# Kernel tuning notes

Measured on AMD Instinct MI355X. Metric: run time of the kernel, lower is better.

Reference implementation:

```python
import jax, jax.numpy as jnp
import numpy as np

INF = 1e10
B, SQ, SK, D = 4, 2048, 2048, 1024


def setup_inputs() -> dict:
    key = jax.random.key(0)
    kq, kk, kv = jax.random.split(key, 3)
    return {
        "query": jax.random.normal(kq, (B, SQ, D), dtype=jnp.float32),
        "key": jax.random.normal(kk, (B, SK, D), dtype=jnp.float32),
        "value": jax.random.normal(kv, (B, SK, D), dtype=jnp.float32),
    }


def reference(query, key, value):
    d_key = query.shape[-1]
    scale = jnp.sqrt(jnp.asarray(d_key, dtype=query.dtype))
    # QK^T: [B, Sq, Sk]
    scores = jnp.einsum("bqd,bkd->bqk", query, key)
    # causal mask: triu(1) * INF over [Sk, Sk], take last Sq rows (matches torch)
    sk = key.shape[1]
    sq = query.shape[1]
    tri = jnp.triu(jnp.full((sk, sk), INF, dtype=scores.dtype), k=1)[-sq:]
    scores = scores - tri[None, :, :]
    # note: mask applied BEFORE scaling, as in the original
    probs = jax.nn.softmax(scores / scale, axis=-1)
    # AV: [B, Sq, D]
    return jnp.einsum("bqk,bkd->bqd", probs, value)
```

## Files before the change

kernel.cpp:

```cpp
#include <hip/hip_runtime.h>
#include <stdint.h>


#define B_SZ 4
#define SEQ 2048
#define DIM 1024
#define QBLK 32
#define KVBLK 128
#define NWAVES 8
#define PAN  ((size_t)DIM * 32)
#define KPAN ((size_t)DIM * 16)

typedef __bf16 bf16x8 __attribute__((ext_vector_type(8)));
typedef unsigned short u16x8 __attribute__((ext_vector_type(8)));
typedef unsigned short u16x4 __attribute__((ext_vector_type(4)));
typedef float f32x4 __attribute__((ext_vector_type(4)));

__device__ __forceinline__ unsigned short f2bf(float f) {
  union { float f; uint32_t u; } c; c.f = f;
  uint32_t u = c.u;
  u += 0x7FFFu + ((u >> 16) & 1u);
  return (unsigned short)(u >> 16);
}

__global__ void transpose_k_kernel(const float* __restrict__ in,
                                   unsigned short* __restrict__ out) {
  const int b   = blockIdx.z;
  const int kv0 = blockIdx.y * 16;
  const int d0  = blockIdx.x * 128;
  const int t   = threadIdx.x;
  const int kvl = t >> 4;
  const int uu  = t & 15;
  const int d   = d0 + uu * 8;
  const float* src = in + (size_t)b * SEQ * DIM + (size_t)(kv0 + kvl) * DIM + d;
  f32x4 a = *(const f32x4*)(src);
  f32x4 c = *(const f32x4*)(src + 4);
  u16x8 pk;
#pragma unroll
  for (int j = 0; j < 4; ++j) { pk[j] = f2bf(a[j]); pk[4 + j] = f2bf(c[j]); }
  *(u16x8*)(out + (size_t)b * SEQ * DIM + (size_t)blockIdx.y * KPAN
            + (size_t)(d >> 3) * 128 + kvl * 8) = pk;
}

__global__ void transpose_v_kernel(const float* __restrict__ in,
                                   unsigned short* __restrict__ out) {
  __shared__ unsigned short tile[32][33];
  const int b  = blockIdx.z;
  const int s0 = blockIdx.y * 32;
  const int d0 = blockIdx.x * 32;
  const int t  = threadIdx.x;
  const int r  = t >> 3;
  const int c4 = (t & 7) * 4;
  const size_t ibase = (size_t)b * SEQ * DIM;
  const size_t obase = (size_t)b * DIM * SEQ;

  f32x4 v = *(const f32x4*)(in + ibase + (size_t)(s0 + r) * DIM + d0 + c4);
#pragma unroll
  for (int j = 0; j < 4; ++j) tile[r][c4 + j] = f2bf(v[j]);
  __syncthreads();
  u16x4 o;
#pragma unroll
  for (int j = 0; j < 4; ++j) o[j] = tile[c4 + j][r];
  *(u16x4*)(out + obase + (size_t)(s0 >> 5) * PAN + (size_t)(d0 + r) * 32 + c4) = o;
}

__device__ __forceinline__ int imin(int a, int b) { return a < b ? a : b; }

__global__ __launch_bounds__(512, 2) void attn_part(
    const float* __restrict__ Qf, const unsigned short* __restrict__ Kp,
    const unsigned short* __restrict__ Vp, float* __restrict__ Out,
    float* __restrict__ Opart, float* __restrict__ Ml, int mode) {
  const int tid  = threadIdx.x;
  const int lane = tid & 63;
  const int wv   = tid >> 6;
  const int g    = lane >> 4;
  const int i16  = lane & 15;
  const int swz  = i16 & 7;

  const int IPX = (mode == 2) ? 80 : (mode == 1) ? 48 : 32;
  const int IPB = (mode == 2) ? 160 : (mode == 1) ? 96 : 64;
  const int item  = (blockIdx.x & 7) * IPX + (blockIdx.x >> 3);
  const int batch = item / IPB;
  const int r     = IPB - 1 - (item % IPB);

  int qt, kvlo, kvhi, slot;
  if (mode == 2) {
    if (r < 16)       { qt = r;             kvlo = 0;    kvhi = 32 * qt + 32;             slot = -1; }
    else if (r < 64)  { qt = r;             kvlo = 0;    kvhi = 512;                      slot = batch * 144 + (r - 16); }
    else if (r < 112) { qt = 16 + (r - 64); kvlo = 512;  kvhi = imin(1024, 32 * qt + 32); slot = batch * 144 + (r - 16); }
    else if (r < 144) { qt = 32 + (r - 112); kvlo = 1024; kvhi = imin(1536, 32 * qt + 32); slot = batch * 144 + (r - 16); }
    else              { qt = 48 + (r - 144); kvlo = 1536; kvhi = 32 * qt + 32;            slot = batch * 144 + (r - 16); }
  } else if (mode == 1) {
    if (r < 32)       { qt = r;             kvlo = 0;    kvhi = 32 * qt + 32;  slot = -1; }
    else if (r < 64)  { qt = 32 + (r - 32); kvlo = 0;    kvhi = 1024;          slot = batch * 64 + (r - 32); }
    else              { qt = 32 + (r - 64); kvlo = 1024; kvhi = 32 * qt + 32;  slot = batch * 64 + (r - 32); }
  } else {
    qt = r; kvlo = 0; kvhi = 32 * qt + 32; slot = -1;
  }

  const int q0 = qt * QBLK;
  const size_t boff = (size_t)batch * SEQ * DIM;

  __shared__ __align__(16) unsigned short Qs[QBLK * 1024];
  __shared__ __align__(16) unsigned short Pl[QBLK * KVBLK];
  __shared__ float pmaxT[QBLK][12];
  __shared__ float psumT[QBLK][12];

  {
    const int row = tid >> 4;
    const int s0  = tid & 15;
    const float* qrow = Qf + boff + (size_t)(q0 + row) * DIM;
#pragma unroll
    for (int k = 0; k < 8; ++k) {
      const int slot2 = s0 + 16 * k;
      f32x4 a = *(const f32x4*)(qrow + slot2 * 8);
      f32x4 b = *(const f32x4*)(qrow + slot2 * 8 + 4);
      u16x8 pk;
#pragma unroll
      for (int j = 0; j < 4; ++j) { pk[j] = f2bf(a[j]); pk[4 + j] = f2bf(b[j]); }
      *(u16x8*)(Qs + row * 1024 + (slot2 ^ (row & 7)) * 8) = pk;
    }
  }

  const f32x4 zero4 = {0.f, 0.f, 0.f, 0.f};
  f32x4 o_acc[8][2];
#pragma unroll
  for (int mt = 0; mt < 8; ++mt)
#pragma unroll
    for (int nt = 0; nt < 2; ++nt) o_acc[mt][nt] = zero4;

  float m_reg[2] = {-1e30f, -1e30f};
  float l_reg[2] = {0.f, 0.f};

  const int ntiles = (kvhi - kvlo + KVBLK - 1) >> 7;
  const unsigned short* kb = Kp + boff + (size_t)wv * KPAN + i16 * 8;
  const unsigned short* vb = Vp + boff + (size_t)(wv * 128 + i16) * 32 + g * 8;

  __syncthreads();

  for (int t = 0; t < ntiles; ++t) {
    const int kv0 = kvlo + t * KVBLK;
    const unsigned short* kt = kb + (size_t)(kv0 >> 4) * KPAN;
    const size_t vt0 = (size_t)(kv0 >> 5) * PAN;

    f32x4 sacc[2];
    sacc[0] = zero4; sacc[1] = zero4;
    bf16x8 vV0[8], vV1[8], vV2[8], vV3[8];

#pragma unroll
    for (int c = 0; c < 8; ++c) {
      if (c == 0) {
#pragma unroll
        for (int mt = 0; mt < 8; ++mt) {
          vV0[mt] = __builtin_bit_cast(bf16x8,
              *(const u16x8*)(vb + vt0 + (size_t)mt * 512));
          vV1[mt] = __builtin_bit_cast(bf16x8,
              *(const u16x8*)(vb + vt0 + PAN + (size_t)mt * 512));
        }
      }
      const unsigned short* qrb0 = Qs + (0 * 16 + i16) * 1024;
      const unsigned short* qrb1 = Qs + (1 * 16 + i16) * 1024;
      bf16x8 kf[4], qf0[4], qf1[4];
#pragma unroll
      for (int kk = 0; kk < 4; ++kk) {
        kf[kk]  = __builtin_bit_cast(bf16x8,
            *(const u16x8*)(kt + (size_t)(c * 16 + kk * 4 + g) * 128));
        qf0[kk] = __builtin_bit_cast(bf16x8, *(const u16x8*)(qrb0 + ((c * 16 + kk * 4 + g) ^ swz) * 8));
        qf1[kk] = __builtin_bit_cast(bf16x8, *(const u16x8*)(qrb1 + ((c * 16 + kk * 4 + g) ^ swz) * 8));
      }
      __builtin_amdgcn_s_setprio(1);
#pragma unroll
      for (int kk = 0; kk < 4; ++kk) {
        sacc[0] = __builtin_amdgcn_mfma_f32_16x16x32_bf16(kf[kk], qf0[kk], sacc[0], 0, 0, 0);
        sacc[1] = __builtin_amdgcn_mfma_f32_16x16x32_bf16(kf[kk], qf1[kk], sacc[1], 0, 0, 0);
      }
      __builtin_amdgcn_s_setprio(0);
    }

    float pm[2];
#pragma unroll
    for (int nt = 0; nt < 2; ++nt) {
      const int qg = q0 + nt * 16 + i16;
      const int kvbase = kv0 + wv * 16 + g * 4;
#pragma unroll
      for (int j = 0; j < 4; ++j) {
        const bool valid = (kvbase + j) <= qg;
        sacc[nt][j] = valid ? sacc[nt][j] * 0.03125f : -1e30f;
      }
      float v = fmaxf(fmaxf(sacc[nt][0], sacc[nt][1]), fmaxf(sacc[nt][2], sacc[nt][3]));
      v = fmaxf(v, __shfl_xor(v, 16));
      v = fmaxf(v, __shfl_xor(v, 32));
      pm[nt] = v;
    }
    if (lane < 32) pmaxT[(lane >> 4) * 16 + (lane & 15)][wv] = (lane < 16) ? pm[0] : pm[1];
    __syncthreads();

    float alpha[2];
#pragma unroll
    for (int nt = 0; nt < 2; ++nt) {
      const float* pr = &pmaxT[nt * 16 + i16][0];
      f32x4 a = *(const f32x4*)(pr);
      f32x4 b = *(const f32x4*)(pr + 4);
      float mx = fmaxf(fmaxf(fmaxf(a[0], a[1]), fmaxf(a[2], a[3])),
                       fmaxf(fmaxf(b[0], b[1]), fmaxf(b[2], b[3])));
      const float m_new = fmaxf(m_reg[nt], mx);
      alpha[nt] = __expf(m_reg[nt] - m_new);
      m_reg[nt] = m_new;

      float ps = 0.f;
      u16x4 pw;
#pragma unroll
      for (int j = 0; j < 4; ++j) {
        const float p = __expf(sacc[nt][j] - m_new);
        ps += p;
        pw[j] = f2bf(p);
      }
      const int pslot = (wv * 2 + (g >> 1)) ^ swz;
      *(u16x4*)(Pl + (nt * 16 + i16) * 128 + pslot * 8 + (g & 1) * 4) = pw;
      ps += __shfl_xor(ps, 16);
      ps += __shfl_xor(ps, 32);
      pm[nt] = ps;
    }
    if (lane < 32) psumT[(lane >> 4) * 16 + (lane & 15)][wv] = (lane < 16) ? pm[0] : pm[1];
    __syncthreads();

#pragma unroll
    for (int nt = 0; nt < 2; ++nt) {
      const float* pr = &psumT[nt * 16 + i16][0];
      f32x4 a = *(const f32x4*)(pr);
      f32x4 b = *(const f32x4*)(pr + 4);
      const float st = (a[0] + a[1] + a[2] + a[3]) + (b[0] + b[1] + b[2] + b[3]);
      l_reg[nt] = alpha[nt] * l_reg[nt] + st;
#pragma unroll
      for (int mt = 0; mt < 8; ++mt)
#pragma unroll
        for (int j = 0; j < 4; ++j) o_acc[mt][nt][j] *= alpha[nt];
    }

#define PV_STEP(KC, VREG)                                                      \
    do {                                                                        \
      bf16x8 pfa = __builtin_bit_cast(bf16x8, *(const u16x8*)(                  \
          Pl + (0 * 16 + i16) * 128 + (((KC) * 4 + g) ^ swz) * 8));             \
      bf16x8 pfb = __builtin_bit_cast(bf16x8, *(const u16x8*)(                  \
          Pl + (1 * 16 + i16) * 128 + (((KC) * 4 + g) ^ swz) * 8));             \
      __builtin_amdgcn_s_setprio(1);                                            \
      _Pragma("unroll")                                                         \
      for (int mt = 0; mt < 8; ++mt) {                                          \
        o_acc[mt][0] = __builtin_amdgcn_mfma_f32_16x16x32_bf16(VREG[mt], pfa,   \
                                                               o_acc[mt][0], 0, 0, 0); \
        o_acc[mt][1] = __builtin_amdgcn_mfma_f32_16x16x32_bf16(VREG[mt], pfb,   \
                                                               o_acc[mt][1], 0, 0, 0); \
      }                                                                         \
      __builtin_amdgcn_s_setprio(0);                                            \
    } while (0)

#pragma unroll
    for (int mt = 0; mt < 8; ++mt)
      vV2[mt] = __builtin_bit_cast(bf16x8,
          *(const u16x8*)(vb + vt0 + 2 * PAN + (size_t)mt * 512));
    PV_STEP(0, vV0);
#pragma unroll
    for (int mt = 0; mt < 8; ++mt)
      vV3[mt] = __builtin_bit_cast(bf16x8,
          *(const u16x8*)(vb + vt0 + 3 * PAN + (size_t)mt * 512));
    PV_STEP(1, vV1);
    PV_STEP(2, vV2);
    PV_STEP(3, vV3);
#undef PV_STEP
  }

  if (slot < 0) {
#pragma unroll
    for (int nt = 0; nt < 2; ++nt) {
      const float linv = 1.f / l_reg[nt];
      const size_t qoff = boff + (size_t)(q0 + nt * 16 + i16) * DIM + wv * 128 + g * 4;
#pragma unroll
      for (int mt = 0; mt < 8; ++mt) {
        f32x4 o;
#pragma unroll
        for (int j = 0; j < 4; ++j) o[j] = o_acc[mt][nt][j] * linv;
        *(f32x4*)(Out + qoff + mt * 16) = o;
      }
    }
  } else {
    const size_t pbase = (size_t)slot * (QBLK * DIM);
#pragma unroll
    for (int nt = 0; nt < 2; ++nt) {
      const size_t qoff = pbase + (size_t)(nt * 16 + i16) * DIM + wv * 128 + g * 4;
#pragma unroll
      for (int mt = 0; mt < 8; ++mt)
        *(f32x4*)(Opart + qoff + mt * 16) = o_acc[mt][nt];
    }
    if (wv == 0 && lane < 16) {
#pragma unroll
      for (int nt = 0; nt < 2; ++nt) {
        Ml[(size_t)slot * 64 + (nt * 16 + lane) * 2 + 0] = m_reg[nt];
        Ml[(size_t)slot * 64 + (nt * 16 + lane) * 2 + 1] = l_reg[nt];
      }
    }
  }
}

__global__ __launch_bounds__(1024) void combine_kernel(
    const float* __restrict__ Opart, const float* __restrict__ Ml,
    float* __restrict__ Out, int mode) {
  const int NT  = (mode == 2) ? 48 : 32;
  const int qt0 = (mode == 2) ? 16 : 32;
  const int b   = blockIdx.x / NT;
  const int qt  = qt0 + blockIdx.x % NT;
  const int n   = (mode == 2) ? ((qt >> 4) + 1) : 2;

  int slots[4];
  if (mode == 2) {
    slots[0] = b * 144 + (qt - 16);
    slots[1] = b * 144 + 48 + (qt - 16);
    slots[2] = b * 144 + 96 + (qt - 32);
    slots[3] = b * 144 + 128 + (qt - 48);
  } else {
    slots[0] = b * 64 + (qt - 32);
    slots[1] = b * 64 + 32 + (qt - 32);
    slots[2] = slots[3] = 0;
  }

  __shared__ float wsh[4][32];
  __shared__ float lsh[32];
  const int t = threadIdx.x;
  if (t < 32) {
    float mc[4], lc[4];
    float m = -1e30f;
#pragma unroll 4
    for (int c = 0; c < 4; ++c) {
      if (c < n) {
        mc[c] = Ml[(size_t)slots[c] * 64 + t * 2 + 0];
        lc[c] = Ml[(size_t)slots[c] * 64 + t * 2 + 1];
        m = fmaxf(m, mc[c]);
      }
    }
    float l = 0.f;
#pragma unroll 4
    for (int c = 0; c < 4; ++c) {
      if (c < n) {
        const float w = __expf(mc[c] - m);
        wsh[c][t] = w;
        l += w * lc[c];
      }
    }
    lsh[t] = 1.f / l;
  }
  __syncthreads();

  const size_t obase = ((size_t)b * SEQ + (size_t)qt * 32) * DIM;
#pragma unroll
  for (int k = 0; k < 8; ++k) {
    const int idx = k * 1024 + t;
    const int q   = idx >> 8;
    const int sl  = idx & 255;
    f32x4 acc = {0.f, 0.f, 0.f, 0.f};
#pragma unroll 4
    for (int c = 0; c < 4; ++c) {
      if (c < n) {
        f32x4 x = *(const f32x4*)(Opart + (size_t)slots[c] * (QBLK * DIM)
                                  + (size_t)q * DIM + sl * 4);
        const float w = wsh[c][q];
#pragma unroll
        for (int j = 0; j < 4; ++j) acc[j] += w * x[j];
      }
    }
    const float li = lsh[q];
    f32x4 o;
#pragma unroll
    for (int j = 0; j < 4; ++j) o[j] = acc[j] * li;
    *(f32x4*)(Out + obase + (size_t)q * DIM + sl * 4) = o;
  }
}

__global__ void attn_naive(const float* __restrict__ Q, const float* __restrict__ K,
                           const float* __restrict__ V, float* __restrict__ Out) {
  const int b = blockIdx.y, q = blockIdx.x;
  const int t = threadIdx.x;
  __shared__ float qs[DIM];
  __shared__ float sc[SEQ];
  __shared__ float red[2];
  const size_t boff = (size_t)b * SEQ * DIM;
  for (int d = t; d < DIM; d += 256) qs[d] = Q[boff + (size_t)q * DIM + d];
  __syncthreads();
  const int kvmax = q + 1;
  for (int kv = t; kv < kvmax; kv += 256) {
    const float* kr = K + boff + (size_t)kv * DIM;
    float s = 0.f;
    for (int d = 0; d < DIM; ++d) s += qs[d] * kr[d];
    sc[kv] = s * 0.03125f;
  }
  __syncthreads();
  if (t == 0) {
    float m = -1e30f;
    for (int kv = 0; kv < kvmax; ++kv) m = fmaxf(m, sc[kv]);
    red[0] = m;
  }
  __syncthreads();
  const float m = red[0];
  for (int kv = t; kv < kvmax; kv += 256) sc[kv] = __expf(sc[kv] - m);
  __syncthreads();
  if (t == 0) {
    float l = 0.f;
    for (int kv = 0; kv < kvmax; ++kv) l += sc[kv];
    red[1] = l;
  }
  __syncthreads();
  const float linv = 1.f / red[1];
  for (int d = t; d < DIM; d += 256) {
    float o = 0.f;
    for (int kv = 0; kv < kvmax; ++kv) o += sc[kv] * V[boff + (size_t)kv * DIM + d];
    Out[boff + (size_t)q * DIM + d] = o * linv;
  }
}

extern "C" void kernel_launch(void* const* d_in, const int* in_sizes, int n_in,
                              void* d_out, int out_size, void* d_ws, size_t ws_size,
                              hipStream_t stream) {
  (void)in_sizes; (void)n_in; (void)out_size;
  const float* Q = (const float*)d_in[0];
  const float* K = (const float*)d_in[1];
  const float* V = (const float*)d_in[2];
  float* Out = (float*)d_out;

  const size_t nelem   = (size_t)B_SZ * SEQ * DIM;
  const size_t bf_b    = nelem * sizeof(unsigned short);
  const size_t ml_b    = (size_t)640 * 64 * sizeof(float);
  const size_t part1_b = (size_t)256 * QBLK * DIM * sizeof(float);
  const size_t part2_b = (size_t)576 * QBLK * DIM * sizeof(float);

  const size_t need0 = 2 * bf_b;
  const size_t need1 = 2 * bf_b + ml_b + part1_b;
  const size_t need2 = 2 * bf_b + ml_b + part2_b;

  const int mode = (ws_size >= need2) ? 2 : (ws_size >= need1) ? 1
                   : (ws_size >= need0) ? 0 : -1;

  if (mode < 0) {
    hipLaunchKernelGGL(attn_naive, dim3(SEQ, B_SZ), dim3(256), 0, stream, Q, K, V, Out);
    return;
  }

  unsigned short* Kp = (unsigned short*)d_ws;
  unsigned short* Vp = Kp + nelem;
  float* Ml    = (float*)(Vp + nelem);
  float* Opart = Ml + 640 * 64;

  hipLaunchKernelGGL(transpose_k_kernel, dim3(DIM / 128, SEQ / 16, B_SZ), dim3(256),
                     0, stream, K, Kp);
  hipLaunchKernelGGL(transpose_v_kernel, dim3(DIM / 32, SEQ / 32, B_SZ), dim3(256),
                     0, stream, V, Vp);

  const int grid = (mode == 2) ? 640 : (mode == 1) ? 384 : 256;
  hipLaunchKernelGGL(attn_part, dim3(grid), dim3(NWAVES * 64), 0, stream,
                     Q, Kp, Vp, Out, Opart, Ml, mode);

  if (mode >= 1) {
    const int cgrid = (mode == 2) ? (B_SZ * 48) : (B_SZ * 32);
    hipLaunchKernelGGL(combine_kernel, dim3(cgrid), dim3(1024), 0, stream,
                       Opart, Ml, Out, mode);
  }
}
```

Baseline: 124.9 us.

## Split attention work across 16 waves per block instead of 8

Doubles the waves per workgroup to 16. Each wave now computes QK^T for a single 16-row query half (h) and one of 8 KV slices, and owns 64 output columns instead of 128 for the PV product. This halves per-wave accumulator and V register footprint, which is meant to raise occupancy and latency hiding. The cost is duplicated K-fragment loads across the two halves and more waves contending at each barrier. V register double-buffering is also reorganized into two reused buffers.

```diff
diff --git a/kernel.cpp b/kernel.cpp
--- a/kernel.cpp
+++ b/kernel.cpp
@@ -7,7 +7,7 @@
 #define DIM 1024
 #define QBLK 32
 #define KVBLK 128
-#define NWAVES 8
+#define NWAVES 16
 #define PAN  ((size_t)DIM * 32)
 #define KPAN ((size_t)DIM * 16)
 
@@ -66,13 +66,15 @@
 
 __device__ __forceinline__ int imin(int a, int b) { return a < b ? a : b; }
 
-__global__ __launch_bounds__(512, 2) void attn_part(
+__global__ __launch_bounds__(1024, 4) void attn_part(
     const float* __restrict__ Qf, const unsigned short* __restrict__ Kp,
     const unsigned short* __restrict__ Vp, float* __restrict__ Out,
     float* __restrict__ Opart, float* __restrict__ Ml, int mode) {
   const int tid  = threadIdx.x;
   const int lane = tid & 63;
   const int wv   = tid >> 6;
+  const int s8   = wv & 7;
+  const int h    = wv >> 3;
   const int g    = lane >> 4;
   const int i16  = lane & 15;
   const int swz  = i16 & 7;
@@ -107,12 +109,12 @@
   __shared__ float psumT[QBLK][12];
 
   {
-    const int row = tid >> 4;
-    const int s0  = tid & 15;
+    const int row = tid >> 5;
+    const int s0  = tid & 31;
     const float* qrow = Qf + boff + (size_t)(q0 + row) * DIM;
 #pragma unroll
-    for (int k = 0; k < 8; ++k) {
-      const int slot2 = s0 + 16 * k;
+    for (int k = 0; k < 4; ++k) {
+      const int slot2 = s0 + 32 * k;
       f32x4 a = *(const f32x4*)(qrow + slot2 * 8);
       f32x4 b = *(const f32x4*)(qrow + slot2 * 8 + 4);
       u16x8 pk;
@@ -123,9 +125,9 @@
   }
 
   const f32x4 zero4 = {0.f, 0.f, 0.f, 0.f};
-  f32x4 o_acc[8][2];
-#pragma unroll
-  for (int mt = 0; mt < 8; ++mt)
+  f32x4 o_acc[4][2];
+#pragma unroll
+  for (int mt = 0; mt < 4; ++mt)
 #pragma unroll
     for (int nt = 0; nt < 2; ++nt) o_acc[mt][nt] = zero4;
 
@@ -133,8 +135,8 @@
   float l_reg[2] = {0.f, 0.f};
 
   const int ntiles = (kvhi - kvlo + KVBLK - 1) >> 7;
-  const unsigned short* kb = Kp + boff + (size_t)wv * KPAN + i16 * 8;
-  const unsigned short* vb = Vp + boff + (size_t)(wv * 128 + i16) * 32 + g * 8;
+  const unsigned short* kb = Kp + boff + (size_t)s8 * KPAN + i16 * 8;
+  const unsigned short* vb = Vp + boff + (size_t)(wv * 64 + i16) * 32 + g * 8;
 
   __syncthreads();
 
@@ -143,56 +145,49 @@
     const unsigned short* kt = kb + (size_t)(kv0 >> 4) * KPAN;
     const size_t vt0 = (size_t)(kv0 >> 5) * PAN;
 
-    f32x4 sacc[2];
-    sacc[0] = zero4; sacc[1] = zero4;
-    bf16x8 vV0[8], vV1[8], vV2[8], vV3[8];
+    f32x4 sacc = zero4;
+    bf16x8 vA[4], vB[4];
 
 #pragma unroll
     for (int c = 0; c < 8; ++c) {
       if (c == 0) {
 #pragma unroll
-        for (int mt = 0; mt < 8; ++mt) {
-          vV0[mt] = __builtin_bit_cast(bf16x8,
+        for (int mt = 0; mt < 4; ++mt) {
+          vA[mt] = __builtin_bit_cast(bf16x8,
               *(const u16x8*)(vb + vt0 + (size_t)mt * 512));
-          vV1[mt] = __builtin_bit_cast(bf16x8,
+          vB[mt] = __builtin_bit_cast(bf16x8,
               *(const u16x8*)(vb + vt0 + PAN + (size_t)mt * 512));
         }
       }
-      const unsigned short* qrb0 = Qs + (0 * 16 + i16) * 1024;
-      const unsigned short* qrb1 = Qs + (1 * 16 + i16) * 1024;
-      bf16x8 kf[4], qf0[4], qf1[4];
+      const unsigned short* qrb = Qs + (h * 16 + i16) * 1024;
+      bf16x8 kf[4], qf[4];
 #pragma unroll
       for (int kk = 0; kk < 4; ++kk) {
-        kf[kk]  = __builtin_bit_cast(bf16x8,
+        kf[kk] = __builtin_bit_cast(bf16x8,
             *(const u16x8*)(kt + (size_t)(c * 16 + kk * 4 + g) * 128));
-        qf0[kk] = __builtin_bit_cast(bf16x8, *(const u16x8*)(qrb0 + ((c * 16 + kk * 4 + g) ^ swz) * 8));
-        qf1[kk] = __builtin_bit_cast(bf16x8, *(const u16x8*)(qrb1 + ((c * 16 + kk * 4 + g) ^ swz) * 8));
+        qf[kk] = __builtin_bit_cast(bf16x8,
+            *(const u16x8*)(qrb + ((c * 16 + kk * 4 + g) ^ swz) * 8));
       }
       __builtin_amdgcn_s_setprio(1);
 #pragma unroll
-      for (int kk = 0; kk < 4; ++kk) {
-        sacc[0] = __builtin_amdgcn_mfma_f32_16x16x32_bf16(kf[kk], qf0[kk], sacc[0], 0, 0, 0);
-        sacc[1] = __builtin_amdgcn_mfma_f32_16x16x32_bf16(kf[kk], qf1[kk], sacc[1], 0, 0, 0);
-      }
+      for (int kk = 0; kk < 4; ++kk)
+        sacc = __builtin_amdgcn_mfma_f32_16x16x32_bf16(kf[kk], qf[kk], sacc, 0, 0, 0);
       __builtin_amdgcn_s_setprio(0);
     }
 
-    float pm[2];
-#pragma unroll
-    for (int nt = 0; nt < 2; ++nt) {
-      const int qg = q0 + nt * 16 + i16;
-      const int kvbase = kv0 + wv * 16 + g * 4;
+    {
+      const int qg = q0 + h * 16 + i16;
+      const int kvbase = kv0 + s8 * 16 + g * 4;
 #pragma unroll
       for (int j = 0; j < 4; ++j) {
         const bool valid = (kvbase + j) <= qg;
-        sacc[nt][j] = valid ? sacc[nt][j] * 0.03125f : -1e30f;
-      }
-      float v = fmaxf(fmaxf(sacc[nt][0], sacc[nt][1]), fmaxf(sacc[nt][2], sacc[nt][3]));
-      v = fmaxf(v, __shfl_xor(v, 16));
-      v = fmaxf(v, __shfl_xor(v, 32));
-      pm[nt] = v;
-    }
-    if (lane < 32) pmaxT[(lane >> 4) * 16 + (lane & 15)][wv] = (lane < 16) ? pm[0] : pm[1];
+        sacc[j] = valid ? sacc[j] * 0.03125f : -1e30f;
+      }
+      float pm = fmaxf(fmaxf(sacc[0], sacc[1]), fmaxf(sacc[2], sacc[3]));
+      pm = fmaxf(pm, __shfl_xor(pm, 16));
+      pm = fmaxf(pm, __shfl_xor(pm, 32));
+      if (lane < 16) pmaxT[h * 16 + lane][s8] = pm;
+    }
     __syncthreads();
 
     float alpha[2];
@@ -206,22 +201,22 @@
       const float m_new = fmaxf(m_reg[nt], mx);
       alpha[nt] = __expf(m_reg[nt] - m_new);
       m_reg[nt] = m_new;
-
+    }
+    {
       float ps = 0.f;
       u16x4 pw;
 #pragma unroll
       for (int j = 0; j < 4; ++j) {
-        const float p = __expf(sacc[nt][j] - m_new);
+        const float p = __expf(sacc[j] - m_reg[h]);
         ps += p;
         pw[j] = f2bf(p);
       }
-      const int pslot = (wv * 2 + (g >> 1)) ^ swz;
-      *(u16x4*)(Pl + (nt * 16 + i16) * 128 + pslot * 8 + (g & 1) * 4) = pw;
+      const int pslot = (s8 * 2 + (g >> 1)) ^ swz;
+      *(u16x4*)(Pl + (h * 16 + i16) * 128 + pslot * 8 + (g & 1) * 4) = pw;
       ps += __shfl_xor(ps, 16);
       ps += __shfl_xor(ps, 32);
-      pm[nt] = ps;
-    }
-    if (lane < 32) psumT[(lane >> 4) * 16 + (lane & 15)][wv] = (lane < 16) ? pm[0] : pm[1];
+      if (lane < 16) psumT[h * 16 + lane][s8] = ps;
+    }
     __syncthreads();
 
 #pragma unroll
@@ -232,7 +227,7 @@
       const float st = (a[0] + a[1] + a[2] + a[3]) + (b[0] + b[1] + b[2] + b[3]);
       l_reg[nt] = alpha[nt] * l_reg[nt] + st;
 #pragma unroll
-      for (int mt = 0; mt < 8; ++mt)
+      for (int mt = 0; mt < 4; ++mt)
 #pragma unroll
         for (int j = 0; j < 4; ++j) o_acc[mt][nt][j] *= alpha[nt];
     }
@@ -245,7 +240,7 @@
           Pl + (1 * 16 + i16) * 128 + (((KC) * 4 + g) ^ swz) * 8));             \
       __builtin_amdgcn_s_setprio(1);                                            \
       _Pragma("unroll")                                                         \
-      for (int mt = 0; mt < 8; ++mt) {                                          \
+      for (int mt = 0; mt < 4; ++mt) {                                          \
         o_acc[mt][0] = __builtin_amdgcn_mfma_f32_16x16x32_bf16(VREG[mt], pfa,   \
                                                                o_acc[mt][0], 0, 0, 0); \
         o_acc[mt][1] = __builtin_amdgcn_mfma_f32_16x16x32_bf16(VREG[mt], pfb,   \
@@ -254,18 +249,18 @@
       __builtin_amdgcn_s_setprio(0);                                            \
     } while (0)
 
-#pragma unroll
-    for (int mt = 0; mt < 8; ++mt)
-      vV2[mt] = __builtin_bit_cast(bf16x8,
+    PV_STEP(0, vA);
+#pragma unroll
+    for (int mt = 0; mt < 4; ++mt)
+      vA[mt] = __builtin_bit_cast(bf16x8,
           *(const u16x8*)(vb + vt0 + 2 * PAN + (size_t)mt * 512));
-    PV_STEP(0, vV0);
-#pragma unroll
-    for (int mt = 0; mt < 8; ++mt)
-      vV3[mt] = __builtin_bit_cast(bf16x8,
+    PV_STEP(1, vB);
+#pragma unroll
+    for (int mt = 0; mt < 4; ++mt)
+      vB[mt] = __builtin_bit_cast(bf16x8,
           *(const u16x8*)(vb + vt0 + 3 * PAN + (size_t)mt * 512));
-    PV_STEP(1, vV1);
-    PV_STEP(2, vV2);
-    PV_STEP(3, vV3);
+    PV_STEP(2, vA);
+    PV_STEP(3, vB);
 #undef PV_STEP
   }
 
@@ -273,9 +268,9 @@
 #pragma unroll
     for (int nt = 0; nt < 2; ++nt) {
       const float linv = 1.f / l_reg[nt];
-      const size_t qoff = boff + (size_t)(q0 + nt * 16 + i16) * DIM + wv * 128 + g * 4;
-#pragma unroll
-      for (int mt = 0; mt < 8; ++mt) {
+      const size_t qoff = boff + (size_t)(q0 + nt * 16 + i16) * DIM + wv * 64 + g * 4;
+#pragma unroll
+      for (int mt = 0; mt < 4; ++mt) {
         f32x4 o;
 #pragma unroll
         for (int j = 0; j < 4; ++j) o[j] = o_acc[mt][nt][j] * linv;
@@ -286,9 +281,9 @@
     const size_t pbase = (size_t)slot * (QBLK * DIM);
 #pragma unroll
     for (int nt = 0; nt < 2; ++nt) {
-      const size_t qoff = pbase + (size_t)(nt * 16 + i16) * DIM + wv * 128 + g * 4;
-#pragma unroll
-      for (int mt = 0; mt < 8; ++mt)
+      const size_t qoff = pbase + (size_t)(nt * 16 + i16) * DIM + wv * 64 + g * 4;
+#pragma unroll
+      for (int mt = 0; mt < 4; ++mt)
         *(f32x4*)(Opart + qoff + mt * 16) = o_acc[mt][nt];
     }
     if (wv == 0 && lane < 16) {
```

Measured after the change: 221.0 us. +77.0%, slower.

## Use 64-row query tiles with uniform 256-wide KV split chunks and bf16 partials

Applied to the files above, without the earlier changes.

Doubles the query tile to 64 rows so each loaded K/V fragment feeds four MFMA column groups instead of two, halving K/V global traffic per query. The KV range is split into fixed 256-wide chunks for query tiles 8 and up (132 chunks per batch plus 8 unsplit tiles), replacing the mode-dependent schedule and its workspace-size fallbacks. Partial outputs are stored as bf16 to reduce combine traffic. The trade-offs are higher register and LDS pressure from the doubled accumulators, reduced precision in partials, and a grid of 560 blocks with a different load-balance profile.

```diff
diff --git a/kernel.cpp b/kernel.cpp
--- a/kernel.cpp
+++ b/kernel.cpp
@@ -5,11 +5,13 @@
 #define B_SZ 4
 #define SEQ 2048
 #define DIM 1024
-#define QBLK 32
+#define QBLK 64
 #define KVBLK 128
 #define NWAVES 8
 #define PAN  ((size_t)DIM * 32)
 #define KPAN ((size_t)DIM * 16)
+#define NCHUNK 132
+#define SLOTSZ 65536
 
 typedef __bf16 bf16x8 __attribute__((ext_vector_type(8)));
 typedef unsigned short u16x8 __attribute__((ext_vector_type(8)));
@@ -69,7 +71,7 @@
 __global__ __launch_bounds__(512, 2) void attn_part(
     const float* __restrict__ Qf, const unsigned short* __restrict__ Kp,
     const unsigned short* __restrict__ Vp, float* __restrict__ Out,
-    float* __restrict__ Opart, float* __restrict__ Ml, int mode) {
+    unsigned short* __restrict__ Opart, float* __restrict__ Ml) {
   const int tid  = threadIdx.x;
   const int lane = tid & 63;
   const int wv   = tid >> 6;
@@ -77,25 +79,17 @@
   const int i16  = lane & 15;
   const int swz  = i16 & 7;
 
-  const int IPX = (mode == 2) ? 80 : (mode == 1) ? 48 : 32;
-  const int IPB = (mode == 2) ? 160 : (mode == 1) ? 96 : 64;
-  const int item  = (blockIdx.x & 7) * IPX + (blockIdx.x >> 3);
-  const int batch = item / IPB;
-  const int r     = IPB - 1 - (item % IPB);
-
+  const int bid   = blockIdx.x;
+  const int batch = bid & 3;
+  const int r     = bid >> 2;
   int qt, kvlo, kvhi, slot;
-  if (mode == 2) {
-    if (r < 16)       { qt = r;             kvlo = 0;    kvhi = 32 * qt + 32;             slot = -1; }
-    else if (r < 64)  { qt = r;             kvlo = 0;    kvhi = 512;                      slot = batch * 144 + (r - 16); }
-    else if (r < 112) { qt = 16 + (r - 64); kvlo = 512;  kvhi = imin(1024, 32 * qt + 32); slot = batch * 144 + (r - 16); }
-    else if (r < 144) { qt = 32 + (r - 112); kvlo = 1024; kvhi = imin(1536, 32 * qt + 32); slot = batch * 144 + (r - 16); }
-    else              { qt = 48 + (r - 144); kvlo = 1536; kvhi = 32 * qt + 32;            slot = batch * 144 + (r - 16); }
-  } else if (mode == 1) {
-    if (r < 32)       { qt = r;             kvlo = 0;    kvhi = 32 * qt + 32;  slot = -1; }
-    else if (r < 64)  { qt = 32 + (r - 32); kvlo = 0;    kvhi = 1024;          slot = batch * 64 + (r - 32); }
-    else              { qt = 32 + (r - 64); kvlo = 1024; kvhi = 32 * qt + 32;  slot = batch * 64 + (r - 32); }
+  if (r < NCHUNK) {
+    int rr = r, q = 31;
+    for (; q >= 8; --q) { const int nc = (q + 4) >> 2; if (rr < nc) break; rr -= nc; }
+    qt = q; kvlo = rr * 256; kvhi = imin(kvlo + 256, 64 * qt + 64);
+    slot = batch * NCHUNK + r;
   } else {
-    qt = r; kvlo = 0; kvhi = 32 * qt + 32; slot = -1;
+    qt = r - NCHUNK; kvlo = 0; kvhi = 64 * qt + 64; slot = -1;
   }
 
   const int q0 = qt * QBLK;
@@ -107,12 +101,12 @@
   __shared__ float psumT[QBLK][12];
 
   {
-    const int row = tid >> 4;
-    const int s0  = tid & 15;
+    const int row = tid >> 3;
+    const int s0  = tid & 7;
     const float* qrow = Qf + boff + (size_t)(q0 + row) * DIM;
 #pragma unroll
-    for (int k = 0; k < 8; ++k) {
-      const int slot2 = s0 + 16 * k;
+    for (int k = 0; k < 16; ++k) {
+      const int slot2 = s0 + 8 * k;
       f32x4 a = *(const f32x4*)(qrow + slot2 * 8);
       f32x4 b = *(const f32x4*)(qrow + slot2 * 8 + 4);
       u16x8 pk;
@@ -123,14 +117,14 @@
   }
 
   const f32x4 zero4 = {0.f, 0.f, 0.f, 0.f};
-  f32x4 o_acc[8][2];
+  f32x4 o_acc[8][4];
 #pragma unroll
   for (int mt = 0; mt < 8; ++mt)
 #pragma unroll
-    for (int nt = 0; nt < 2; ++nt) o_acc[mt][nt] = zero4;
-
-  float m_reg[2] = {-1e30f, -1e30f};
-  float l_reg[2] = {0.f, 0.f};
+    for (int nt = 0; nt < 4; ++nt) o_acc[mt][nt] = zero4;
+
+  float m_reg[4] = {-1e30f, -1e30f, -1e30f, -1e30f};
+  float l_reg[4] = {0.f, 0.f, 0.f, 0.f};
 
   const int ntiles = (kvhi - kvlo + KVBLK - 1) >> 7;
   const unsigned short* kb = Kp + boff + (size_t)wv * KPAN + i16 * 8;
@@ -143,43 +137,43 @@
     const unsigned short* kt = kb + (size_t)(kv0 >> 4) * KPAN;
     const size_t vt0 = (size_t)(kv0 >> 5) * PAN;
 
-    f32x4 sacc[2];
-    sacc[0] = zero4; sacc[1] = zero4;
-    bf16x8 vV0[8], vV1[8], vV2[8], vV3[8];
+    f32x4 sacc[4];
+#pragma unroll
+    for (int nt = 0; nt < 4; ++nt) sacc[nt] = zero4;
+    bf16x8 vV[8];
 
 #pragma unroll
     for (int c = 0; c < 8; ++c) {
       if (c == 0) {
 #pragma unroll
-        for (int mt = 0; mt < 8; ++mt) {
-          vV0[mt] = __builtin_bit_cast(bf16x8,
+        for (int mt = 0; mt < 8; ++mt)
+          vV[mt] = __builtin_bit_cast(bf16x8,
               *(const u16x8*)(vb + vt0 + (size_t)mt * 512));
-          vV1[mt] = __builtin_bit_cast(bf16x8,
-              *(const u16x8*)(vb + vt0 + PAN + (size_t)mt * 512));
-        }
-      }
-      const unsigned short* qrb0 = Qs + (0 * 16 + i16) * 1024;
-      const unsigned short* qrb1 = Qs + (1 * 16 + i16) * 1024;
-      bf16x8 kf[4], qf0[4], qf1[4];
-#pragma unroll
-      for (int kk = 0; kk < 4; ++kk) {
-        kf[kk]  = __builtin_bit_cast(bf16x8,
+      }
+      bf16x8 kf[4];
+#pragma unroll
+      for (int kk = 0; kk < 4; ++kk)
+        kf[kk] = __builtin_bit_cast(bf16x8,
             *(const u16x8*)(kt + (size_t)(c * 16 + kk * 4 + g) * 128));
-        qf0[kk] = __builtin_bit_cast(bf16x8, *(const u16x8*)(qrb0 + ((c * 16 + kk * 4 + g) ^ swz) * 8));
-        qf1[kk] = __builtin_bit_cast(bf16x8, *(const u16x8*)(qrb1 + ((c * 16 + kk * 4 + g) ^ swz) * 8));
-      }
-      __builtin_amdgcn_s_setprio(1);
-#pragma unroll
-      for (int kk = 0; kk < 4; ++kk) {
-        sacc[0] = __builtin_amdgcn_mfma_f32_16x16x32_bf16(kf[kk], qf0[kk], sacc[0], 0, 0, 0);
-        sacc[1] = __builtin_amdgcn_mfma_f32_16x16x32_bf16(kf[kk], qf1[kk], sacc[1], 0, 0, 0);
-      }
-      __builtin_amdgcn_s_setprio(0);
-    }
-
-    float pm[2];
-#pragma unroll
-    for (int nt = 0; nt < 2; ++nt) {
+#pragma unroll
+      for (int nt = 0; nt < 4; ++nt) {
+        const unsigned short* qrb = Qs + (nt * 16 + i16) * 1024;
+        bf16x8 qf[4];
+#pragma unroll
+        for (int kk = 0; kk < 4; ++kk)
+          qf[kk] = __builtin_bit_cast(bf16x8,
+              *(const u16x8*)(qrb + ((c * 16 + kk * 4 + g) ^ swz) * 8));
+        __builtin_amdgcn_s_setprio(1);
+#pragma unroll
+        for (int kk = 0; kk < 4; ++kk)
+          sacc[nt] = __builtin_amdgcn_mfma_f32_16x16x32_bf16(kf[kk], qf[kk], sacc[nt], 0, 0, 0);
+        __builtin_amdgcn_s_setprio(0);
+      }
+    }
+
+    float pm[4];
+#pragma unroll
+    for (int nt = 0; nt < 4; ++nt) {
       const int qg = q0 + nt * 16 + i16;
       const int kvbase = kv0 + wv * 16 + g * 4;
 #pragma unroll
@@ -192,12 +186,15 @@
       v = fmaxf(v, __shfl_xor(v, 32));
       pm[nt] = v;
     }
-    if (lane < 32) pmaxT[(lane >> 4) * 16 + (lane & 15)][wv] = (lane < 16) ? pm[0] : pm[1];
+    if (lane < 16) {
+#pragma unroll
+      for (int nt = 0; nt < 4; ++nt) pmaxT[nt * 16 + lane][wv] = pm[nt];
+    }
     __syncthreads();
 
-    float alpha[2];
-#pragma unroll
-    for (int nt = 0; nt < 2; ++nt) {
+    float alpha[4];
+#pragma unroll
+    for (int nt = 0; nt < 4; ++nt) {
       const float* pr = &pmaxT[nt * 16 + i16][0];
       f32x4 a = *(const f32x4*)(pr);
       f32x4 b = *(const f32x4*)(pr + 4);
@@ -221,11 +218,14 @@
       ps += __shfl_xor(ps, 32);
       pm[nt] = ps;
     }
-    if (lane < 32) psumT[(lane >> 4) * 16 + (lane & 15)][wv] = (lane < 16) ? pm[0] : pm[1];
+    if (lane < 16) {
+#pragma unroll
+      for (int nt = 0; nt < 4; ++nt) psumT[nt * 16 + lane][wv] = pm[nt];
+    }
     __syncthreads();
 
 #pragma unroll
-    for (int nt = 0; nt < 2; ++nt) {
+    for (int nt = 0; nt < 4; ++nt) {
       const float* pr = &psumT[nt * 16 + i16][0];
       f32x4 a = *(const f32x4*)(pr);
       f32x4 b = *(const f32x4*)(pr + 4);
@@ -237,41 +237,31 @@
         for (int j = 0; j < 4; ++j) o_acc[mt][nt][j] *= alpha[nt];
     }
 
-#define PV_STEP(KC, VREG)                                                      \
-    do {                                                                        \
-      bf16x8 pfa = __builtin_bit_cast(bf16x8, *(const u16x8*)(                  \
-          Pl + (0 * 16 + i16) * 128 + (((KC) * 4 + g) ^ swz) * 8));             \
-      bf16x8 pfb = __builtin_bit_cast(bf16x8, *(const u16x8*)(                  \
-          Pl + (1 * 16 + i16) * 128 + (((KC) * 4 + g) ^ swz) * 8));             \
-      __builtin_amdgcn_s_setprio(1);                                            \
-      _Pragma("unroll")                                                         \
-      for (int mt = 0; mt < 8; ++mt) {                                          \
-        o_acc[mt][0] = __builtin_amdgcn_mfma_f32_16x16x32_bf16(VREG[mt], pfa,   \
-                                                               o_acc[mt][0], 0, 0, 0); \
-        o_acc[mt][1] = __builtin_amdgcn_mfma_f32_16x16x32_bf16(VREG[mt], pfb,   \
-                                                               o_acc[mt][1], 0, 0, 0); \
-      }                                                                         \
-      __builtin_amdgcn_s_setprio(0);                                            \
-    } while (0)
-
-#pragma unroll
-    for (int mt = 0; mt < 8; ++mt)
-      vV2[mt] = __builtin_bit_cast(bf16x8,
-          *(const u16x8*)(vb + vt0 + 2 * PAN + (size_t)mt * 512));
-    PV_STEP(0, vV0);
-#pragma unroll
-    for (int mt = 0; mt < 8; ++mt)
-      vV3[mt] = __builtin_bit_cast(bf16x8,
-          *(const u16x8*)(vb + vt0 + 3 * PAN + (size_t)mt * 512));
-    PV_STEP(1, vV1);
-    PV_STEP(2, vV2);
-    PV_STEP(3, vV3);
-#undef PV_STEP
+#pragma unroll
+    for (int kc = 0; kc < 4; ++kc) {
+      if (kc > 0) {
+#pragma unroll
+        for (int mt = 0; mt < 8; ++mt)
+          vV[mt] = __builtin_bit_cast(bf16x8,
+              *(const u16x8*)(vb + vt0 + (size_t)kc * PAN + (size_t)mt * 512));
+      }
+#pragma unroll
+      for (int nt = 0; nt < 4; ++nt) {
+        bf16x8 pf = __builtin_bit_cast(bf16x8, *(const u16x8*)(
+            Pl + (nt * 16 + i16) * 128 + (((kc * 4 + g) ^ swz) * 8)));
+        __builtin_amdgcn_s_setprio(1);
+#pragma unroll
+        for (int mt = 0; mt < 8; ++mt)
+          o_acc[mt][nt] = __builtin_amdgcn_mfma_f32_16x16x32_bf16(vV[mt], pf,
+                                                                  o_acc[mt][nt], 0, 0, 0);
+        __builtin_amdgcn_s_setprio(0);
+      }
+    }
   }
 
   if (slot < 0) {
 #pragma unroll
-    for (int nt = 0; nt < 2; ++nt) {
+    for (int nt = 0; nt < 4; ++nt) {
       const float linv = 1.f / l_reg[nt];
       const size_t qoff = boff + (size_t)(q0 + nt * 16 + i16) * DIM + wv * 128 + g * 4;
 #pragma unroll
@@ -283,87 +273,73 @@
       }
     }
   } else {
-    const size_t pbase = (size_t)slot * (QBLK * DIM);
-#pragma unroll
-    for (int nt = 0; nt < 2; ++nt) {
-      const size_t qoff = pbase + (size_t)(nt * 16 + i16) * DIM + wv * 128 + g * 4;
-#pragma unroll
-      for (int mt = 0; mt < 8; ++mt)
-        *(f32x4*)(Opart + qoff + mt * 16) = o_acc[mt][nt];
+    unsigned short* op = Opart + (size_t)slot * SLOTSZ;
+#pragma unroll
+    for (int nt = 0; nt < 4; ++nt) {
+#pragma unroll
+      for (int mt = 0; mt < 8; ++mt) {
+        u16x4 pw;
+#pragma unroll
+        for (int j = 0; j < 4; ++j) pw[j] = f2bf(o_acc[mt][nt][j]);
+        *(u16x4*)(op + (size_t)(nt * 16 + i16) * 1024 + wv * 128 + mt * 16 + g * 4) = pw;
+      }
     }
     if (wv == 0 && lane < 16) {
 #pragma unroll
-      for (int nt = 0; nt < 2; ++nt) {
-        Ml[(size_t)slot * 64 + (nt * 16 + lane) * 2 + 0] = m_reg[nt];
-        Ml[(size_t)slot * 64 + (nt * 16 + lane) * 2 + 1] = l_reg[nt];
+      for (int nt = 0; nt < 4; ++nt) {
+        Ml[(size_t)slot * 128 + (nt * 16 + lane) * 2 + 0] = m_reg[nt];
+        Ml[(size_t)slot * 128 + (nt * 16 + lane) * 2 + 1] = l_reg[nt];
       }
     }
   }
 }
 
 __global__ __launch_bounds__(1024) void combine_kernel(
-    const float* __restrict__ Opart, const float* __restrict__ Ml,
-    float* __restrict__ Out, int mode) {
-  const int NT  = (mode == 2) ? 48 : 32;
-  const int qt0 = (mode == 2) ? 16 : 32;
-  const int b   = blockIdx.x / NT;
-  const int qt  = qt0 + blockIdx.x % NT;
-  const int n   = (mode == 2) ? ((qt >> 4) + 1) : 2;
-
-  int slots[4];
-  if (mode == 2) {
-    slots[0] = b * 144 + (qt - 16);
-    slots[1] = b * 144 + 48 + (qt - 16);
-    slots[2] = b * 144 + 96 + (qt - 32);
-    slots[3] = b * 144 + 128 + (qt - 48);
-  } else {
-    slots[0] = b * 64 + (qt - 32);
-    slots[1] = b * 64 + 32 + (qt - 32);
-    slots[2] = slots[3] = 0;
-  }
-
-  __shared__ float wsh[4][32];
-  __shared__ float lsh[32];
+    const unsigned short* __restrict__ Opart, const float* __restrict__ Ml,
+    float* __restrict__ Out) {
+  const int b  = blockIdx.x & 3;
+  const int qt = 8 + (blockIdx.x >> 2);
+  int rbase = 0;
+  for (int q = 31; q > qt; --q) rbase += (q + 4) >> 2;
+  const int n = (qt + 4) >> 2;
+  const int sbase = b * NCHUNK + rbase;
+
+  __shared__ float wsh[8][64];
+  __shared__ float lsh[64];
   const int t = threadIdx.x;
-  if (t < 32) {
-    float mc[4], lc[4];
+  if (t < 64) {
+    float mc[8], lc[8];
     float m = -1e30f;
-#pragma unroll 4
-    for (int c = 0; c < 4; ++c) {
-      if (c < n) {
-        mc[c] = Ml[(size_t)slots[c] * 64 + t * 2 + 0];
-        lc[c] = Ml[(size_t)slots[c] * 64 + t * 2 + 1];
-        m = fmaxf(m, mc[c]);
-      }
+    for (int c = 0; c < n; ++c) {
+      mc[c] = Ml[(size_t)(sbase + c) * 128 + t * 2 + 0];
+      lc[c] = Ml[(size_t)(sbase + c) * 128 + t * 2 + 1];
+      m = fmaxf(m, mc[c]);
     }
     float l = 0.f;
-#pragma unroll 4
-    for (int c = 0; c < 4; ++c) {
-      if (c < n) {
-        const float w = __expf(mc[c] - m);
-        wsh[c][t] = w;
-        l += w * lc[c];
-      }
+    for (int c = 0; c < n; ++c) {
+      const float w = __expf(mc[c] - m);
+      wsh[c][t] = w;
+      l += w * lc[c];
     }
     lsh[t] = 1.f / l;
   }
   __syncthreads();
 
-  const size_t obase = ((size_t)b * SEQ + (size_t)qt * 32) * DIM;
-#pragma unroll
-  for (int k = 0; k < 8; ++k) {
+  const size_t obase = ((size_t)b * SEQ + (size_t)qt * 64) * DIM;
+#pragma unroll
+  for (int k = 0; k < 16; ++k) {
     const int idx = k * 1024 + t;
     const int q   = idx >> 8;
     const int sl  = idx & 255;
     f32x4 acc = {0.f, 0.f, 0.f, 0.f};
-#pragma unroll 4
-    for (int c = 0; c < 4; ++c) {
-      if (c < n) {
-        f32x4 x = *(const f32x4*)(Opart + (size_t)slots[c] * (QBLK * DIM)
-                                  + (size_t)q * DIM + sl * 4);
-        const float w = wsh[c][q];
-#pragma unroll
-        for (int j = 0; j < 4; ++j) acc[j] += w * x[j];
+    for (int c = 0; c < n; ++c) {
+      u16x4 x = *(const u16x4*)(Opart + (size_t)(sbase + c) * SLOTSZ
+                                + (size_t)q * 1024 + sl * 4);
+      const float w = wsh[c][q];
+#pragma unroll
+      for (int j = 0; j < 4; ++j) {
+        union { float f; uint32_t u; } cv; cv.u = ((uint32_t)x[j]) << 16;
+        acc[j] += w * cv.f;
       }
     }
     const float li = lsh[q];
@@ -424,41 +400,31 @@
   const float* V = (const float*)d_in[2];
   float* Out = (float*)d_out;
 
-  const size_t nelem   = (size_t)B_SZ * SEQ * DIM;
-  const size_t bf_b    = nelem * sizeof(unsigned short);
-  const size_t ml_b    = (size_t)640 * 64 * sizeof(float);
-  const size_t part1_b = (size_t)256 * QBLK * DIM * sizeof(float);
-  const size_t part2_b = (size_t)576 * QBLK * DIM * sizeof(float);
-
-  const size_t need0 = 2 * bf_b;
-  const size_t need1 = 2 * bf_b + ml_b + part1_b;
-  const size_t need2 = 2 * bf_b + ml_b + part2_b;
-
-  const int mode = (ws_size >= need2) ? 2 : (ws_size >= need1) ? 1
-                   : (ws_size >= need0) ? 0 : -1;
-
-  if (mode < 0) {
+  const size_t nelem  = (size_t)B_SZ * SEQ * DIM;
+  const size_t bf_b   = nelem * sizeof(unsigned short);
+  const size_t nslots = (size_t)B_SZ * NCHUNK;
+  const size_t ml_b   = nslots * 128 * sizeof(float);
+  const size_t op_b   = nslots * SLOTSZ * sizeof(unsigned short);
+  const size_t need   = 2 * bf_b + ml_b + op_b;
+
+  if (ws_size < need) {
     hipLaunchKernelGGL(attn_naive, dim3(SEQ, B_SZ), dim3(256), 0, stream, Q, K, V, Out);
     return;
   }
 
   unsigned short* Kp = (unsigned short*)d_ws;
   unsigned short* Vp = Kp + nelem;
-  float* Ml    = (float*)(Vp + nelem);
-  float* Opart = Ml + 640 * 64;
+  float* Ml = (float*)(Vp + nelem);
+  unsigned short* Opart = (unsigned short*)(Ml + nslots * 128);
 
   hipLaunchKernelGGL(transpose_k_kernel, dim3(DIM / 128, SEQ / 16, B_SZ), dim3(256),
                      0, stream, K, Kp);
   hipLaunchKernelGGL(transpose_v_kernel, dim3(DIM / 32, SEQ / 32, B_SZ), dim3(256),
                      0, stream, V, Vp);
 
-  const int grid = (mode == 2) ? 640 : (mode == 1) ? 384 : 256;
-  hipLaunchKernelGGL(attn_part, dim3(grid), dim3(NWAVES * 64), 0, stream,
-                     Q, Kp, Vp, Out, Opart, Ml, mode);
-
-  if (mode >= 1) {
-    const int cgrid = (mode == 2) ? (B_SZ * 48) : (B_SZ * 32);
-    hipLaunchKernelGGL(combine_kernel, dim3(cgrid), dim3(1024), 0, stream,
-                       Opart, Ml, Out, mode);
-  }
-}
+  hipLaunchKernelGGL(attn_part, dim3(B_SZ * (NCHUNK + 8)), dim3(NWAVES * 64),
+                     0, stream, Q, Kp, Vp, Out, Opart, Ml);
+
+  hipLaunchKernelGGL(combine_kernel, dim3(B_SZ * 24), dim3(1024), 0, stream,
+                     Opart, Ml, Out);
+}
```

Result: slower. 206.0 us (+65.0%).
